# Kernel tuning notes

Measured on AMD Instinct MI355X. Metric: run time of the kernel, lower is better.

## Reference

```python
import jax, jax.numpy as jnp
import numpy as np

NSIDE = 64
LMAX = 96
MMAX = 96
NLAT = 4 * NSIDE - 1
B, C = 4, 64


def healpix_nlon_ring(t, nside):
    if 0 <= t < nside - 1:
        return 4 * (t + 1)
    if t <= 3 * nside - 1:
        return 4 * nside
    return 4 * (4 * nside - t - 1)


NLON = [healpix_nlon_ring(t, NSIDE) for t in range(NLAT)]


def healpix_latitude_theta(nside):
    t = np.arange(0, 4 * nside - 1).astype(np.float64)
    z = np.zeros_like(t)
    m1 = t < nside - 1
    m2 = (t >= nside - 1) & (t <= 3 * nside - 1)
    m3 = (t > 3 * nside - 1) & (t <= 4 * nside - 2)
    z[m1] = 1 - (t[m1] + 1) ** 2 / (3 * nside ** 2)
    z[m2] = 4 / 3 - 2 * (t[m2] + 1) / (3 * nside)
    z[m3] = (4 * nside - 1 - t[m3]) ** 2 / (3 * nside ** 2) - 1
    return np.arccos(z)


def healpix_longitude_offset(mmax, nside):
    t = np.arange(0, 4 * nside - 1).astype(np.float64)
    shift = 0.5
    tt = np.zeros_like(t)
    tt = np.where((t + 1 >= nside) & (t + 1 <= 3 * nside), shift * ((t - nside + 2) % 2) * np.pi / (2 * nside), tt)
    tt = np.where(t + 1 > 3 * nside, shift * np.pi / (2 * (4 * nside - t - 1)), tt)
    tt = np.where(t + 1 < nside, shift * np.pi / (2 * (t + 1)), tt)
    return np.einsum('t,m->tm', tt, np.arange(0, mmax).astype(np.float64))


def legpoly(mmax, lmax, x, norm='ortho', inverse=False, csphase=True):
    # (-1)^m c^l_m P^l_m(x), shape (mmax, lmax, len(x)); faithful numpy copy
    nmax = max(mmax, lmax)
    vdm = np.zeros((nmax, nmax, len(x)), dtype=np.float64)
    norm_factor = 1.0 if norm == 'ortho' else np.sqrt(4 * np.pi)
    norm_factor = 1.0 / norm_factor if inverse else norm_factor
    vdm[0, 0, :] = norm_factor / np.sqrt(4 * np.pi)
    for n in range(1, nmax):
        vdm[n - 1, n, :] = np.sqrt(2 * n + 1) * x * vdm[n - 1, n - 1, :]
        vdm[n, n, :] = np.sqrt((2 * n + 1) * (1 + x) * (1 - x) / 2 / n) * vdm[n - 1, n - 1, :]
    for n in range(2, nmax):
        for m in range(0, n - 1):
            vdm[m, n, :] = (x * np.sqrt((2 * n - 1) / (n - m) * (2 * n + 1) / (n + m)) * vdm[m, n - 1, :]
                            - np.sqrt((n + m - 1) / (n - m) * (2 * n + 1) / (2 * n - 3) * (n - m - 1) / (n + m)) * vdm[m, n - 2, :])
    if norm == 'schmidt':
        for num in range(0, nmax):
            if inverse:
                vdm[:, num, :] = vdm[:, num, :] * np.sqrt(2 * num + 1)
            else:
                vdm[:, num, :] = vdm[:, num, :] / np.sqrt(2 * num + 1)
    vdm = vdm[:mmax, :lmax]
    if csphase:
        vdm[1::2] *= -1
    return vdm


def setup_inputs() -> dict:
    key = jax.random.key(0)
    k1, k2 = jax.random.split(key)
    x_real = jax.random.normal(k1, (B, C, LMAX, MMAX), dtype=jnp.float32)
    x_imag = jax.random.normal(k2, (B, C, LMAX, MMAX), dtype=jnp.float32)
    theta = healpix_latitude_theta(NSIDE)
    pct = legpoly(MMAX, LMAX, np.cos(theta), norm='ortho', inverse=True, csphase=True)  # (M, L, NLAT)
    offset = healpix_longitude_offset(MMAX, NSIDE)  # (NLAT, M)
    return {
        'x_real': x_real,
        'x_imag': x_imag,
        'pct': jnp.asarray(pct, dtype=jnp.float32),
        'offset': jnp.asarray(offset, dtype=jnp.float32),
    }


def reference(x_real, x_imag, pct, offset):
    # Legendre transform: (..., l, m) x (m, l, k) -> (..., k=nlat, m)
    rl = jnp.einsum('...lm,mlk->...km', x_real, pct)
    im = jnp.einsum('...lm,mlk->...km', x_imag, pct)
    x = (rl + 1j * im) * jnp.exp(1j * offset)  # (..., NLAT, MMAX) complex64
    # ragged per-ring irfft: group rings sharing the same nlon into one batched irfft
    groups = {}
    for t, n in enumerate(NLON):
        groups.setdefault(n, []).append(t)
    ring_out = [None] * NLAT
    for n, idxs in groups.items():
        y = jnp.fft.irfft(x[..., jnp.asarray(idxs), :], n=n, axis=-1, norm='forward')  # (..., g, n)
        for i, t in enumerate(idxs):
            ring_out[t] = y[..., i, :]
    return jnp.concatenate(ring_out, axis=-1)  # (..., 12*nside^2)
```

## Files before the change

kernel.cpp:

```cpp
#include <hip/hip_runtime.h>
#include <hip/hip_bf16.h>
#include <math.h>

#define NLAT 255
#define NPIX 49152
#define PI_F 3.14159265358979323846f

typedef _Float16 half_t;
typedef half_t half8 __attribute__((ext_vector_type(8)));
typedef float  f32x4 __attribute__((ext_vector_type(4)));

__device__ __forceinline__ void ring_params(int t, int& n, int& roff) {
    if (t < 63)        { n = 4 * (t + 1); roff = 2 * t * (t + 1); }
    else if (t <= 191) { n = 256;         roff = 8064 + 256 * (t - 63); }
    else               { int w = 255 - t; n = 4 * w; roff = 49152 - 2 * w * (w + 1); }
}

__device__ __forceinline__ float ring_alpha(int t) {
    return (t < 63)   ? PI_F / (4.0f * (float)(t + 1))
         : (t <= 191) ? ((((t - 62) & 1)) ? PI_F / 256.0f : 0.0f)
         :              PI_F / (4.0f * (float)(255 - t));
}

__global__ __launch_bounds__(256) void k_prep(
        const float* __restrict__ pct,
        const float* __restrict__ xr, const float* __restrict__ xi,
        half_t* __restrict__ pctT, half_t* __restrict__ xh) {
    __shared__ float smem[96 * 33];
    const int bx  = blockIdx.x;
    const int tid = threadIdx.x;

    if (bx < 768) {
        const int m = bx >> 3, t0 = (bx & 7) * 32;
        for (int idx = tid; idx < 96 * 32; idx += 256) {
            int l = idx >> 5, tt = idx & 31, t = t0 + tt;
            smem[l * 33 + tt] = (t < NLAT) ? pct[((size_t)m * 96 + l) * NLAT + t] : 0.f;
        }
        __syncthreads();
        for (int idx = tid; idx < 96 * 32; idx += 256) {
            int tt = idx / 96, l = idx - tt * 96;
            pctT[((size_t)m * 256 + t0 + tt) * 96 + l] = (half_t)smem[l * 33 + tt];
        }
    } else {
        const int id  = bx - 768;
        const int z   = id / 768;
        const int rem = id - z * 768;
        const int l   = rem % 96;
        const int bc0 = (rem / 96) * 32;
        const int comp = z / 3, m0 = (z % 3) * 32;
        const float* in = comp ? xi : xr;
        const int tx = tid & 31, ty = tid >> 5;
#pragma unroll
        for (int j = 0; j < 4; ++j) {
            int bcl = ty + j * 8;
            smem[bcl * 33 + tx] = in[((size_t)(bc0 + bcl) * 96 + l) * 96 + m0 + tx];
        }
        __syncthreads();
#pragma unroll
        for (int j = 0; j < 4; ++j) {
            int ml = ty + j * 8;
            xh[((((size_t)(comp * 96 + m0 + ml)) * 12 + (l >> 3)) * 256 + bc0 + tx) * 8
               + (l & 7)] = (half_t)smem[tx * 33 + ml];
        }
    }
}

__global__ __launch_bounds__(256) void k_leg(
        const half_t* __restrict__ pctT, const half_t* __restrict__ xh,
        half_t* __restrict__ Xp) {
    const int mg  = blockIdx.x;
    const int t0  = blockIdx.y * 64;
    const int bc0 = blockIdx.z * 32;
    const int wid = threadIdx.x >> 6, lane = threadIdx.x & 63;
    const int wm = wid & 1, wn = wid >> 1;
    const int row = lane & 15, quad = lane >> 4;
    const int tbase = t0 + wm * 32;
    const int bc    = bc0 + wn * 16 + row;

    f32x4 acc[4][2][2];
#pragma unroll
    for (int a = 0; a < 4; ++a)
#pragma unroll
        for (int b = 0; b < 2; ++b)
#pragma unroll
            for (int d = 0; d < 2; ++d) acc[a][b][d] = (f32x4)0.f;

#pragma unroll
    for (int k0 = 0; k0 < 96; k0 += 32) {
        const int kA = k0 + quad * 8;
        half8 af[4][2], bf[4][2];
#pragma unroll
        for (int mi = 0; mi < 4; ++mi) {
            const int m = mg * 4 + mi;
#pragma unroll
            for (int mt = 0; mt < 2; ++mt)
                af[mi][mt] = *(const half8*)(pctT +
                    ((size_t)m * 256 + tbase + mt * 16 + row) * 96 + kA);
#pragma unroll
            for (int c = 0; c < 2; ++c)
                bf[mi][c] = *(const half8*)(xh +
                    ((((size_t)(c * 96 + m)) * 12 + (k0 >> 3) + quad) * 256 + bc) * 8);
        }
#pragma unroll
        for (int mi = 0; mi < 4; ++mi)
#pragma unroll
            for (int c = 0; c < 2; ++c)
#pragma unroll
                for (int mt = 0; mt < 2; ++mt)
                    acc[mi][c][mt] = __builtin_amdgcn_mfma_f32_16x16x32_f16(
                        af[mi][mt], bf[mi][c], acc[mi][c][mt], 0, 0, 0);
    }

#pragma unroll
    for (int mt = 0; mt < 2; ++mt)
#pragma unroll
        for (int r = 0; r < 4; ++r) {
            const int t = tbase + mt * 16 + quad * 4 + r;
            half8 v;
#pragma unroll
            for (int mi = 0; mi < 4; ++mi) {
                v[2 * mi]     = (half_t)acc[mi][0][mt][r];
                v[2 * mi + 1] = (half_t)acc[mi][1][mt][r];
            }
            *(half8*)(Xp + (((size_t)t * 24 + mg) * 256 + bc) * 8) = v;
        }
}

__global__ __launch_bounds__(256) void k_dft(
        const half_t* __restrict__ Xp, float* __restrict__ out) {
    const int bid = blockIdx.x;
    const int xcd = bid & 7, sub = bid >> 3;
    const int wg  = (xcd < 4 ? xcd * 128 : 512 + (xcd - 4) * 127) + sub;
    const int t   = wg >> 2;
    const int p0  = (wg & 3) * 64;
    int n, roff; ring_params(t, n, roff);
    if (p0 >= n) return;

    const int wid = threadIdx.x >> 6, lane = threadIdx.x & 63;
    const int row = lane & 15, quad = lane >> 4;
    const int mq  = quad * 4;

    const half_t* xpb = Xp + (((size_t)t * 24 + quad) * 256 + wid * 64 + row) * 8;

    const int n2 = n >> 1;
    const int mh = min(95, n2);
    const int ks = (2 * (mh + 1) + 31) >> 5;

    const float alpha = ring_alpha(t);
    const float invn  = 1.0f / (float)n;
    float cc[4], ss[4], d1c[4], d1s[4], d16c[4], d16s[4];
#pragma unroll
    for (int pi = 0; pi < 4; ++pi) {
        float phi = 6.28318530717958647692f * (float)(p0 + pi * 16 + row) * invn
                  + alpha;
        __sincosf(phi, &d1s[pi], &d1c[pi]);
        __sincosf(16.0f * phi, &d16s[pi], &d16c[pi]);
        __sincosf((float)mq * phi, &ss[pi], &cc[pi]);
    }

    f32x4 acc[4][4];
#pragma unroll
    for (int i = 0; i < 4; ++i)
#pragma unroll
        for (int j = 0; j < 4; ++j) acc[i][j] = (f32x4)0.f;

    auto step = [&](int kk) {
        half8 b[4];
#pragma unroll
        for (int bn = 0; bn < 4; ++bn)
            b[bn] = *(const half8*)(xpb + kk * 8192 + bn * 128);
        half8 af[4];
#pragma unroll
        for (int pi = 0; pi < 4; ++pi) {
            float c = cc[pi], s = ss[pi];
            half8 a;
#pragma unroll
            for (int j = 0; j < 4; ++j) {
                int m = kk * 16 + mq + j;
                float sc = (m == 0) ? 1.f : (m < n2) ? 2.f : (m == n2) ? 1.f : 0.f;
                a[2 * j]     = (half_t)(sc * c);
                a[2 * j + 1] = (half_t)(-sc * s);
                float cn = c * d1c[pi] - s * d1s[pi];
                s = s * d1c[pi] + c * d1s[pi];
                c = cn;
            }
            float cn = cc[pi] * d16c[pi] - ss[pi] * d16s[pi];
            ss[pi] = ss[pi] * d16c[pi] + cc[pi] * d16s[pi];
            cc[pi] = cn;
            af[pi] = a;
        }
#pragma unroll
        for (int pi = 0; pi < 4; ++pi)
#pragma unroll
            for (int bn = 0; bn < 4; ++bn)
                acc[pi][bn] = __builtin_amdgcn_mfma_f32_16x16x32_f16(
                    af[pi], b[bn], acc[pi][bn], 0, 0, 0);
    };

    if (ks == 6) {
#pragma unroll
        for (int kk = 0; kk < 6; ++kk) step(kk);
    } else {
        for (int kk = 0; kk < ks; ++kk) step(kk);
    }

#pragma unroll
    for (int pi = 0; pi < 4; ++pi) {
        const int p = p0 + pi * 16 + quad * 4;
        if (p < n) {
#pragma unroll
            for (int bn = 0; bn < 4; ++bn) {
                const int bc = wid * 64 + bn * 16 + row;
                float4 v = make_float4(acc[pi][bn][0], acc[pi][bn][1],
                                       acc[pi][bn][2], acc[pi][bn][3]);
                *(float4*)(out + (size_t)bc * NPIX + roff + p) = v;
            }
        }
    }
}

extern "C" void kernel_launch(void* const* d_in, const int* in_sizes, int n_in,
                              void* d_out, int out_size, void* d_ws, size_t ws_size,
                              hipStream_t stream) {
    const float* xr  = (const float*)d_in[0];
    const float* xi  = (const float*)d_in[1];
    const float* pct = (const float*)d_in[2];
    float* out = (float*)d_out;

    char* ws = (char*)d_ws;
    half_t* pctT = (half_t*)ws;
    half_t* xh   = (half_t*)(ws + 4718592);
    half_t* Xp   = (half_t*)(ws + 4718592 + 9437184);

    k_prep<<<dim3(5376), 256, 0, stream>>>(pct, xr, xi, pctT, xh);
    k_leg <<<dim3(24, 4, 8), 256, 0, stream>>>(pctT, xh, Xp);
    k_dft <<<dim3(1020), 256, 0, stream>>>(Xp, out);
}
```

Baseline: 136.5 us.

## Share DFT twiddle tile across waves via LDS and remap Legendre grid per XCD

k_dft used to have every wave recompute the same twiddle A-fragments with per-lane rotation recurrences. It now builds the twiddle tile once per block in shared memory, computing each entry directly with sincos, and all four waves read it back. This removes redundant ALU work and the accumulated recurrence error, at the cost of a __syncthreads and about 24KB of LDS per block, which may limit occupancy. k_leg also switches to a 1D grid with an XCD-aware block remap, so that blocks sharing an m-group land on the same XCD for L2 reuse.

```diff
diff --git a/kernel.cpp b/kernel.cpp
--- a/kernel.cpp
+++ b/kernel.cpp
@@ -8,6 +8,7 @@
 
 typedef _Float16 half_t;
 typedef half_t half8 __attribute__((ext_vector_type(8)));
+typedef half_t half2_t __attribute__((ext_vector_type(2)));
 typedef float  f32x4 __attribute__((ext_vector_type(4)));
 
 __device__ __forceinline__ void ring_params(int t, int& n, int& roff) {
@@ -68,9 +69,12 @@
 __global__ __launch_bounds__(256) void k_leg(
         const half_t* __restrict__ pctT, const half_t* __restrict__ xh,
         half_t* __restrict__ Xp) {
-    const int mg  = blockIdx.x;
-    const int t0  = blockIdx.y * 64;
-    const int bc0 = blockIdx.z * 32;
+    const int b   = blockIdx.x;
+    const int wg  = (b & 7) * 96 + (b >> 3);
+    const int mg  = wg >> 5;
+    const int rem = wg & 31;
+    const int t0  = (rem >> 3) * 64;
+    const int bc0 = (rem & 7) * 32;
     const int wid = threadIdx.x >> 6, lane = threadIdx.x & 63;
     const int wm = wid & 1, wn = wid >> 1;
     const int row = lane & 15, quad = lane >> 4;
@@ -81,9 +85,9 @@
 #pragma unroll
     for (int a = 0; a < 4; ++a)
 #pragma unroll
-        for (int b = 0; b < 2; ++b)
-#pragma unroll
-            for (int d = 0; d < 2; ++d) acc[a][b][d] = (f32x4)0.f;
+        for (int bb = 0; bb < 2; ++bb)
+#pragma unroll
+            for (int d = 0; d < 2; ++d) acc[a][bb][d] = (f32x4)0.f;
 
 #pragma unroll
     for (int k0 = 0; k0 < 96; k0 += 32) {
@@ -128,6 +132,7 @@
 
 __global__ __launch_bounds__(256) void k_dft(
         const half_t* __restrict__ Xp, float* __restrict__ out) {
+    __shared__ half_t Alds[6 * 4 * 64 * 8];
     const int bid = blockIdx.x;
     const int xcd = bid & 7, sub = bid >> 3;
     const int wg  = (xcd < 4 ? xcd * 128 : 512 + (xcd - 4) * 127) + sub;
@@ -136,27 +141,39 @@
     int n, roff; ring_params(t, n, roff);
     if (p0 >= n) return;
 
-    const int wid = threadIdx.x >> 6, lane = threadIdx.x & 63;
+    const int tid = threadIdx.x;
+    const int wid = tid >> 6, lane = tid & 63;
     const int row = lane & 15, quad = lane >> 4;
-    const int mq  = quad * 4;
-
-    const half_t* xpb = Xp + (((size_t)t * 24 + quad) * 256 + wid * 64 + row) * 8;
 
     const int n2 = n >> 1;
     const int mh = min(95, n2);
     const int ks = (2 * (mh + 1) + 31) >> 5;
 
-    const float alpha = ring_alpha(t);
-    const float invn  = 1.0f / (float)n;
-    float cc[4], ss[4], d1c[4], d1s[4], d16c[4], d16s[4];
-#pragma unroll
-    for (int pi = 0; pi < 4; ++pi) {
-        float phi = 6.28318530717958647692f * (float)(p0 + pi * 16 + row) * invn
-                  + alpha;
-        __sincosf(phi, &d1s[pi], &d1c[pi]);
-        __sincosf(16.0f * phi, &d16s[pi], &d16c[pi]);
-        __sincosf((float)mq * phi, &ss[pi], &cc[pi]);
-    }
+    {
+        const float alpha = ring_alpha(t);
+        const float invn  = 1.0f / (float)n;
+        const int npairs = ks << 10;
+        for (int idx = tid; idx < npairs; idx += 256) {
+            const int mloc = idx & 15;
+            const int prow = (idx >> 4) & 63;
+            const int kk   = idx >> 10;
+            const int m    = kk * 16 + mloc;
+            const float phi = 6.28318530717958647692f * (float)(p0 + prow) * invn
+                            + alpha;
+            const float sc = (m == 0) ? 1.f : (m < n2) ? 2.f : (m == n2) ? 1.f : 0.f;
+            float s, c;
+            __sincosf((float)m * phi, &s, &c);
+            half2_t v; v[0] = (half_t)(sc * c); v[1] = (half_t)(-sc * s);
+            const int pos = (((kk * 4 + (prow >> 4)) * 64
+                             + (mloc >> 2) * 16 + (prow & 15)) * 8
+                             + (mloc & 3) * 2);
+            *(half2_t*)(Alds + pos) = v;
+        }
+    }
+    __syncthreads();
+
+    const half_t* xpb = Xp + (((size_t)t * 24 + quad) * 256 + wid * 64 + row) * 8;
+    const half_t* alb = Alds + (size_t)lane * 8;
 
     f32x4 acc[4][4];
 #pragma unroll
@@ -165,36 +182,19 @@
         for (int j = 0; j < 4; ++j) acc[i][j] = (f32x4)0.f;
 
     auto step = [&](int kk) {
-        half8 b[4];
+        half8 b[4], a[4];
 #pragma unroll
         for (int bn = 0; bn < 4; ++bn)
             b[bn] = *(const half8*)(xpb + kk * 8192 + bn * 128);
-        half8 af[4];
-#pragma unroll
-        for (int pi = 0; pi < 4; ++pi) {
-            float c = cc[pi], s = ss[pi];
-            half8 a;
-#pragma unroll
-            for (int j = 0; j < 4; ++j) {
-                int m = kk * 16 + mq + j;
-                float sc = (m == 0) ? 1.f : (m < n2) ? 2.f : (m == n2) ? 1.f : 0.f;
-                a[2 * j]     = (half_t)(sc * c);
-                a[2 * j + 1] = (half_t)(-sc * s);
-                float cn = c * d1c[pi] - s * d1s[pi];
-                s = s * d1c[pi] + c * d1s[pi];
-                c = cn;
-            }
-            float cn = cc[pi] * d16c[pi] - ss[pi] * d16s[pi];
-            ss[pi] = ss[pi] * d16c[pi] + cc[pi] * d16s[pi];
-            cc[pi] = cn;
-            af[pi] = a;
-        }
+#pragma unroll
+        for (int pi = 0; pi < 4; ++pi)
+            a[pi] = *(const half8*)(alb + (kk * 4 + pi) * 512);
 #pragma unroll
         for (int pi = 0; pi < 4; ++pi)
 #pragma unroll
             for (int bn = 0; bn < 4; ++bn)
                 acc[pi][bn] = __builtin_amdgcn_mfma_f32_16x16x32_f16(
-                    af[pi], b[bn], acc[pi][bn], 0, 0, 0);
+                    a[pi], b[bn], acc[pi][bn], 0, 0, 0);
     };
 
     if (ks == 6) {
@@ -233,6 +233,6 @@
     half_t* Xp   = (half_t*)(ws + 4718592 + 9437184);
 
     k_prep<<<dim3(5376), 256, 0, stream>>>(pct, xr, xi, pctT, xh);
-    k_leg <<<dim3(24, 4, 8), 256, 0, stream>>>(pctT, xh, Xp);
+    k_leg <<<dim3(768), 256, 0, stream>>>(pctT, xh, Xp);
     k_dft <<<dim3(1020), 256, 0, stream>>>(Xp, out);
 }
```

Result: no change. 133.8 us (-1.9%).
